# Kernel optimization log

Hardware: AMD Instinct MI355X
Metric: run time of the kernel (lower is better)

Reference implementation:

```python
import jax, jax.numpy as jnp
import numpy as np

B, LX, LR, D = 16, 2048, 1024, 768
T = LX + LR + 3  # CLS + x + RING + xr + END


def setup_inputs() -> dict:
    key = jax.random.key(0)
    ks = jax.random.split(key, 7)
    X = jax.random.normal(ks[0], (B, LX, D), dtype=jnp.float32)
    Xr = jax.random.normal(ks[1], (B, LR, D), dtype=jnp.float32)
    CLS = jax.random.normal(ks[2], (1, D), dtype=jnp.float32)
    RING = jax.random.normal(ks[3], (1, D), dtype=jnp.float32)
    END = jax.random.normal(ks[4], (1, D), dtype=jnp.float32)
    lx = jax.random.randint(ks[5], (B,), 0, LX, dtype=jnp.int32)
    lr = jax.random.randint(ks[6], (B,), 0, LR, dtype=jnp.int32)
    return {"X": X, "Xr": Xr, "CLS": CLS, "RING": RING, "END": END,
            "lx": lx, "lr": lr}


def reference(X, Xr, CLS, RING, END, lx, lr):
    # Jagged assembly: out[b] = concat([CLS, X[b,:lx[b]], RING, Xr[b,:lr[b]], END])
    # Output is padded to T = LX + LR + 3 with zeros beyond each sample's length.
    t = jnp.arange(T)[None, :]                     # [1, T]
    lxb = lx[:, None].astype(jnp.int32)            # [B, 1]
    lrb = lr[:, None].astype(jnp.int32)

    # Region masks per (b, t)
    is_cls = (t == 0)                              # [B broadcastable, T]
    is_x = (t >= 1) & (t <= lxb)                   # [B, T]
    is_ring = (t == lxb + 1)
    is_xr = (t >= lxb + 2) & (t < lxb + 2 + lrb)
    is_end = (t == lxb + lrb + 2)

    # Gather source tokens (clamped indices; masked out where invalid)
    pos_x = jnp.clip(t - 1, 0, LX - 1)             # [1, T] same for all b
    gx = X[:, pos_x[0], :]                         # [B, T, D]
    pos_xr = jnp.clip(t - lxb - 2, 0, LR - 1)      # [B, T]
    gxr = jnp.take_along_axis(Xr, pos_xr[:, :, None], axis=1)  # [B, T, D]

    out = (is_cls[:, :, None] * CLS[None, :, :]
           + is_ring[:, :, None] * RING[None, :, :]
           + is_end[:, :, None] * END[None, :, :]
           + jnp.where(is_x[:, :, None], gx, 0.0)
           + jnp.where(is_xr[:, :, None], gxr, 0.0))
    return out
```

## Files before the change

### kernel.cpp

```cpp
#include <hip/hip_runtime.h>


constexpr int B_  = 16;
constexpr int LX_ = 2048;
constexpr int LR_ = 1024;
constexpr int D_  = 768;
constexpr int T_  = LX_ + LR_ + 3;
constexpr int RPB = 8;
constexpr int NTL = (T_ + RPB - 1) / RPB;

typedef float vfloat4 __attribute__((ext_vector_type(4)));

__global__ __launch_bounds__(192)
void assemble_rows_kernel(const float* __restrict__ X,
                          const float* __restrict__ Xr,
                          const float* __restrict__ CLS,
                          const float* __restrict__ RING,
                          const float* __restrict__ END,
                          const int* __restrict__ lx,
                          const int* __restrict__ lr,
                          float* __restrict__ out)
{
    const int b   = blockIdx.y;
    const int t0  = blockIdx.x * RPB;
    const int lxb = lx[b];
    const int lrb = lr[b];
    const int doff = threadIdx.x * 4;

    const float* __restrict__ Xb   = X  + ((size_t)b * LX_) * D_ + doff;
    const float* __restrict__ Xrb  = Xr + ((size_t)b * LR_) * D_ + doff;
    float* __restrict__ outp = out + ((size_t)b * T_ + t0) * D_ + doff;

    vfloat4 v[RPB];

    #pragma unroll
    for (int i = 0; i < RPB; ++i) {
        const int t = t0 + i;
        v[i] = (vfloat4)(0.f);
        if (t >= T_) continue;
        if (t == 0) {
            v[i] = *reinterpret_cast<const vfloat4*>(CLS + doff);
        } else if (t <= lxb) {
            v[i] = *reinterpret_cast<const vfloat4*>(Xb + (size_t)(t - 1) * D_);
        } else if (t == lxb + 1) {
            v[i] = *reinterpret_cast<const vfloat4*>(RING + doff);
        } else if (t < lxb + 2 + lrb) {
            v[i] = *reinterpret_cast<const vfloat4*>(Xrb + (size_t)(t - lxb - 2) * D_);
        } else if (t == lxb + lrb + 2) {
            v[i] = *reinterpret_cast<const vfloat4*>(END + doff);
        }
    }

    #pragma unroll
    for (int i = 0; i < RPB; ++i) {
        if (t0 + i < T_) {
            *reinterpret_cast<vfloat4*>(outp + (size_t)i * D_) = v[i];
        }
    }
}

extern "C" void kernel_launch(void* const* d_in, const int* in_sizes, int n_in,
                              void* d_out, int out_size, void* d_ws, size_t ws_size,
                              hipStream_t stream)
{
    const float* X    = (const float*)d_in[0];
    const float* Xr   = (const float*)d_in[1];
    const float* CLS  = (const float*)d_in[2];
    const float* RING = (const float*)d_in[3];
    const float* END  = (const float*)d_in[4];
    const int* lx = (const int*)d_in[5];
    const int* lr = (const int*)d_in[6];
    float* out = (float*)d_out;

    hipLaunchKernelGGL(assemble_rows_kernel, dim3(NTL, B_), dim3(192), 0, stream,
                       X, Xr, CLS, RING, END, lx, lr, out);
}
```

Before: 258.1 us.

## Flatten to grid-stride float4 copy with nontemporal loads and stores

```diff
diff --git a/kernel.cpp b/kernel.cpp
--- a/kernel.cpp
+++ b/kernel.cpp
@@ -6,13 +6,48 @@
 constexpr int LR_ = 1024;
 constexpr int D_  = 768;
 constexpr int T_  = LX_ + LR_ + 3;
-constexpr int RPB = 8;
-constexpr int NTL = (T_ + RPB - 1) / RPB;
+constexpr int D4  = D_ / 4;
+constexpr unsigned NF4 = (unsigned)B_ * T_ * D4;
+constexpr int NBLK = 2048;
+constexpr int NTHR = 256;
 
 typedef float vfloat4 __attribute__((ext_vector_type(4)));
 
-__global__ __launch_bounds__(192)
-void assemble_rows_kernel(const float* __restrict__ X,
+__device__ __forceinline__ vfloat4 route(unsigned i,
+                                         const float* __restrict__ X,
+                                         const float* __restrict__ Xr,
+                                         const float* __restrict__ CLS,
+                                         const float* __restrict__ RING,
+                                         const float* __restrict__ END,
+                                         const int* __restrict__ lx,
+                                         const int* __restrict__ lr)
+{
+    const unsigned row = i / (unsigned)D4;
+    const int doff = (int)(i - row * (unsigned)D4) * 4;
+    const unsigned b = row / (unsigned)T_;
+    const int t = (int)(row - b * (unsigned)T_);
+    const int lxb = lx[b];
+    const int lrb = lr[b];
+
+    vfloat4 v = (vfloat4)(0.f);
+    if (t == 0) {
+        v = *reinterpret_cast<const vfloat4*>(CLS + doff);
+    } else if (t <= lxb) {
+        v = __builtin_nontemporal_load(reinterpret_cast<const vfloat4*>(
+                X + ((size_t)(b * LX_ + (t - 1)) * D_ + doff)));
+    } else if (t == lxb + 1) {
+        v = *reinterpret_cast<const vfloat4*>(RING + doff);
+    } else if (t < lxb + 2 + lrb) {
+        v = __builtin_nontemporal_load(reinterpret_cast<const vfloat4*>(
+                Xr + ((size_t)(b * LR_ + (t - lxb - 2)) * D_ + doff)));
+    } else if (t == lxb + lrb + 2) {
+        v = *reinterpret_cast<const vfloat4*>(END + doff);
+    }
+    return v;
+}
+
+__global__ __launch_bounds__(NTHR)
+void assemble_flat_kernel(const float* __restrict__ X,
                           const float* __restrict__ Xr,
                           const float* __restrict__ CLS,
                           const float* __restrict__ RING,
@@ -21,41 +56,23 @@
                           const int* __restrict__ lr,
                           float* __restrict__ out)
 {
-    const int b   = blockIdx.y;
-    const int t0  = blockIdx.x * RPB;
-    const int lxb = lx[b];
-    const int lrb = lr[b];
-    const int doff = threadIdx.x * 4;
+    const unsigned stride = NBLK * NTHR;
+    unsigned i = blockIdx.x * NTHR + threadIdx.x;
 
-    const float* __restrict__ Xb   = X  + ((size_t)b * LX_) * D_ + doff;
-    const float* __restrict__ Xrb  = Xr + ((size_t)b * LR_) * D_ + doff;
-    float* __restrict__ outp = out + ((size_t)b * T_ + t0) * D_ + doff;
-
-    vfloat4 v[RPB];
-
-    #pragma unroll
-    for (int i = 0; i < RPB; ++i) {
-        const int t = t0 + i;
-        v[i] = (vfloat4)(0.f);
-        if (t >= T_) continue;
-        if (t == 0) {
-            v[i] = *reinterpret_cast<const vfloat4*>(CLS + doff);
-        } else if (t <= lxb) {
-            v[i] = *reinterpret_cast<const vfloat4*>(Xb + (size_t)(t - 1) * D_);
-        } else if (t == lxb + 1) {
-            v[i] = *reinterpret_cast<const vfloat4*>(RING + doff);
-        } else if (t < lxb + 2 + lrb) {
-            v[i] = *reinterpret_cast<const vfloat4*>(Xrb + (size_t)(t - lxb - 2) * D_);
-        } else if (t == lxb + lrb + 2) {
-            v[i] = *reinterpret_cast<const vfloat4*>(END + doff);
-        }
+    while (i + stride < NF4) {
+        vfloat4 v0 = route(i,          X, Xr, CLS, RING, END, lx, lr);
+        vfloat4 v1 = route(i + stride, X, Xr, CLS, RING, END, lx, lr);
+        __builtin_nontemporal_store(v0,
+            reinterpret_cast<vfloat4*>(out + (size_t)i * 4));
+        __builtin_nontemporal_store(v1,
+            reinterpret_cast<vfloat4*>(out + (size_t)(i + stride) * 4));
+        i += 2 * stride;
     }
-
-    #pragma unroll
-    for (int i = 0; i < RPB; ++i) {
-        if (t0 + i < T_) {
-            *reinterpret_cast<vfloat4*>(outp + (size_t)i * D_) = v[i];
-        }
+    while (i < NF4) {
+        vfloat4 v = route(i, X, Xr, CLS, RING, END, lx, lr);
+        __builtin_nontemporal_store(v,
+            reinterpret_cast<vfloat4*>(out + (size_t)i * 4));
+        i += stride;
     }
 }
 
@@ -72,6 +89,6 @@
     const int* lr = (const int*)d_in[6];
     float* out = (float*)d_out;
 
-    hipLaunchKernelGGL(assemble_rows_kernel, dim3(NTL, B_), dim3(192), 0, stream,
+    hipLaunchKernelGGL(assemble_flat_kernel, dim3(NBLK), dim3(NTHR), 0, stream,
                        X, Xr, CLS, RING, END, lx, lr, out);
 }
```

Result: faster. 247.3 us (-4.2%).
